# Kernel tuning notes

Hardware: AMD Instinct MI355X
Metric: run time of the kernel (lower is better)

## Reference

```python
import jax, jax.numpy as jnp
import numpy as np

B, N, D = 8, 2048, 1024

def setup_inputs() -> dict:
    key = jax.random.key(0)
    k1, k2, k3, k4 = jax.random.split(key, 4)
    q = jax.random.normal(k1, (B, N, D), dtype=jnp.float32)
    k = jax.random.normal(k2, (B, N, D), dtype=jnp.float32)
    v = jax.random.uniform(k3, (B, N, N), dtype=jnp.float32)
    # nn.Linear default init (kaiming-uniform-ish); scale is irrelevant for correctness
    bound = 1.0 / np.sqrt(D)
    W1 = jax.random.uniform(k4, (D, D), dtype=jnp.float32, minval=-bound, maxval=bound)
    b1 = jnp.zeros((D,), dtype=jnp.float32)
    return {"q": q, "k": k, "v": v, "W1": W1, "b1": b1}

def adj_normalization(adj):
    # D^{-1/2} A D^{-1/2} with rowsum clamped at 1; expressed as O(N^2)
    # broadcast scaling instead of the original's two diagonal bmms.
    rowsum = jnp.maximum(adj.sum(-1), 1.0)          # [B, N]
    d_inv_sqrt = rowsum ** -0.5                      # [B, N]
    return d_inv_sqrt[:, :, None] * adj * d_inv_sqrt[:, None, :]

def reference(q, k, v, W1, b1):
    # ff_layers == 1: q_out = linear1(q) (dropout is identity in eval);
    # k is unused because _fc returns (q_out, q_out).
    q_out = jnp.einsum('bnd,ed->bne', q, W1) + b1    # [B, N, D]
    attn = jnp.einsum('bnd,bmd->bnm', q_out, q_out)  # [B, N, N]
    # comb_mode == 2 (learn_n_norm): symmetric normalization of attn; v unused.
    output = adj_normalization(attn)
    return (output, attn)
```

## Files before the change

### kernel.cpp

```cpp
#include <hip/hip_runtime.h>

#define B_ 8
#define N_ 2048
#define D_ 1024

using u16 = unsigned short;
typedef __attribute__((ext_vector_type(8))) short short8;
typedef __attribute__((ext_vector_type(4))) float f32x4;
typedef __attribute__((ext_vector_type(4))) float float4v;
typedef __attribute__((ext_vector_type(4))) int int4v;

static __device__ __forceinline__ float bf2f(u16 h) {
  return __uint_as_float(((unsigned)h) << 16);
}
static __device__ __forceinline__ u16 f2bf(float f) {
  unsigned u = __float_as_uint(f);
  u += 0x7FFFu + ((u >> 16) & 1u);
  return (u16)(u >> 16);
}

static __device__ __forceinline__ void gload16(const void* g, void* l) {
  __builtin_amdgcn_global_load_lds((const __attribute__((address_space(1))) void*)g,
                                   (__attribute__((address_space(3))) void*)l, 16, 0, 0);
}


__device__ __forceinline__ void stage(u16* __restrict__ L,
                                      const u16* __restrict__ gA,
                                      const u16* __restrict__ gB,
                                      int kof, int w) {
  #pragma unroll
  for (int i = 0; i < 4; ++i)
    gload16(gA + (size_t)(i * 64) * 1024 + kof, L + i * 4096 + w * 512);
  #pragma unroll
  for (int i = 0; i < 4; ++i)
    gload16(gB + (size_t)(i * 64) * 1024 + kof, L + 16384 + i * 4096 + w * 512);
}

__device__ __forceinline__ void ktile(const u16* __restrict__ Lb,
                                      int wr, int wc, int lane15, int ck0,
                                      f32x4 (&acc)[8][4]) {
  const u16* Ar = Lb + (wr * 128 + lane15) * 64;
  const u16* Br = Lb + 16384 + (wc * 64 + lane15) * 64;
  const int ck1 = ck0 ^ 32;
  short8 a[4], a2[4], b[4];

  #pragma unroll
  for (int m = 0; m < 4; ++m) a[m] = *(const short8*)(Ar + m * 1024 + ck0);
  #pragma unroll
  for (int n = 0; n < 4; ++n) b[n] = *(const short8*)(Br + n * 1024 + ck0);
  __builtin_amdgcn_s_barrier();
  __builtin_amdgcn_s_setprio(1);
  #pragma unroll
  for (int m = 0; m < 4; ++m)
    #pragma unroll
    for (int n = 0; n < 4; ++n)
      acc[m][n] = __builtin_amdgcn_mfma_f32_16x16x32_bf16(a[m], b[n], acc[m][n], 0, 0, 0);
  __builtin_amdgcn_s_setprio(0);
  __builtin_amdgcn_s_barrier();

  #pragma unroll
  for (int m = 0; m < 4; ++m) a2[m] = *(const short8*)(Ar + (m + 4) * 1024 + ck0);
  __builtin_amdgcn_s_barrier();
  __builtin_amdgcn_s_setprio(1);
  #pragma unroll
  for (int m = 0; m < 4; ++m)
    #pragma unroll
    for (int n = 0; n < 4; ++n)
      acc[m + 4][n] = __builtin_amdgcn_mfma_f32_16x16x32_bf16(a2[m], b[n], acc[m + 4][n], 0, 0, 0);
  __builtin_amdgcn_s_setprio(0);
  __builtin_amdgcn_s_barrier();

  #pragma unroll
  for (int m = 0; m < 4; ++m) a[m] = *(const short8*)(Ar + m * 1024 + ck1);
  #pragma unroll
  for (int n = 0; n < 4; ++n) b[n] = *(const short8*)(Br + n * 1024 + ck1);
  __builtin_amdgcn_s_barrier();
  __builtin_amdgcn_s_setprio(1);
  #pragma unroll
  for (int m = 0; m < 4; ++m)
    #pragma unroll
    for (int n = 0; n < 4; ++n)
      acc[m][n] = __builtin_amdgcn_mfma_f32_16x16x32_bf16(a[m], b[n], acc[m][n], 0, 0, 0);
  __builtin_amdgcn_s_setprio(0);
  __builtin_amdgcn_s_barrier();

  #pragma unroll
  for (int m = 0; m < 4; ++m) a2[m] = *(const short8*)(Ar + (m + 4) * 1024 + ck1);
  __builtin_amdgcn_s_barrier();
  __builtin_amdgcn_s_setprio(1);
  #pragma unroll
  for (int m = 0; m < 4; ++m)
    #pragma unroll
    for (int n = 0; n < 4; ++n)
      acc[m + 4][n] = __builtin_amdgcn_mfma_f32_16x16x32_bf16(a2[m], b[n], acc[m + 4][n], 0, 0, 0);
  __builtin_amdgcn_s_setprio(0);
  __builtin_amdgcn_s_barrier();
}

template<int MODE>
__global__ __launch_bounds__(512, 2)
void gemm8p(const u16* __restrict__ Abase, const u16* __restrict__ Bbase,
            const float* __restrict__ aux,
            void* __restrict__ C0, float* __restrict__ C1)
{
  __shared__ u16 lds[2][32768];
  const int tid = threadIdx.x;
  const int w = tid >> 6, l = tid & 63;

  int tm0, tn0, z = 0;
  if (MODE == 0) {
    const int bid = blockIdx.x;
    const int s = (bid & 7) * 32 + (bid >> 3);
    tm0 = (s >> 2) << 8;
    tn0 = (s & 3) << 8;
  } else {
    const int bid = blockIdx.x;
    const int s = (bid & 7) * 64 + (bid >> 3);
    z  = s >> 6;
    tm0 = ((s >> 3) & 7) << 8;
    tn0 = (s & 7) << 8;
  }
  const u16* A  = Abase + (MODE ? (size_t)z * N_ * D_ : 0);
  const u16* Bm = (MODE ? A : Bbase);

  const int sr = w * 8 + (l >> 3);
  const int sc = (((l & 7) ^ (l >> 3)) << 4) >> 1;
  const u16* gA = A  + (size_t)(tm0 + sr) * 1024 + sc;
  const u16* gB = Bm + (size_t)(tn0 + sr) * 1024 + sc;

  const int lane15 = l & 15, lhi = l >> 4;
  const int ck0 = ((lhi << 4) ^ ((l & 7) << 4)) >> 1;
  const int wr = w >> 2, wc = w & 3;

  f32x4 acc[8][4];
  #pragma unroll
  for (int m = 0; m < 8; ++m)
    #pragma unroll
    for (int n = 0; n < 4; ++n)
      acc[m][n] = (f32x4){0.f, 0.f, 0.f, 0.f};

  stage(&lds[0][0], gA, gB, 0, w);
  stage(&lds[1][0], gA, gB, 64, w);

  for (int t = 0; t < 16; t += 2) {
    asm volatile("s_waitcnt vmcnt(8)" ::: "memory");
    __builtin_amdgcn_s_barrier();
    ktile(&lds[0][0], wr, wc, lane15, ck0, acc);
    stage(&lds[0][0], gA, gB, ((t + 2) & 15) * 64, w);
    asm volatile("s_waitcnt vmcnt(8)" ::: "memory");
    __builtin_amdgcn_s_barrier();
    ktile(&lds[1][0], wr, wc, lane15, ck0, acc);
    stage(&lds[1][0], gA, gB, ((t + 3) & 15) * 64, w);
  }
  asm volatile("s_waitcnt vmcnt(0)" ::: "memory");

  const int rbase = tm0 + wr * 128 + lhi * 4;
  const int cbase = tn0 + wc * 64 + lane15;

  if (MODE == 0) {
    u16* C = (u16*)C0;
    #pragma unroll
    for (int m = 0; m < 8; ++m)
      #pragma unroll
      for (int n = 0; n < 4; ++n) {
        const int col = cbase + n * 16;
        const float bv = aux[col];
        #pragma unroll
        for (int j = 0; j < 4; ++j)
          C[(size_t)(rbase + m * 16 + j) * 1024 + col] = f2bf(acc[m][n][j] + bv);
      }
  } else {
    float* Cattn = (float*)C0 + (size_t)z * N_ * N_;
    float* Cout  = C1 + (size_t)z * N_ * N_;
    const float* dv = aux + z * N_;
    float di[8][4];
    #pragma unroll
    for (int m = 0; m < 8; ++m)
      #pragma unroll
      for (int j = 0; j < 4; ++j)
        di[m][j] = dv[rbase + m * 16 + j];
    #pragma unroll
    for (int m = 0; m < 8; ++m)
      #pragma unroll
      for (int n = 0; n < 4; ++n) {
        const int col = cbase + n * 16;
        const float dj = dv[col];
        #pragma unroll
        for (int j = 0; j < 4; ++j) {
          const size_t off = (size_t)(rbase + m * 16 + j) * N_ + col;
          const float a = acc[m][n][j];
          Cattn[off] = a;
          Cout[off]  = a * di[m][j] * dj;
        }
      }
  }
}

__global__ void cvt_q_qsum(const float* __restrict__ q, u16* __restrict__ qbf,
                           float* __restrict__ qsum) {
  const int wi = blockIdx.x * 256 + threadIdx.x;
  const int d0 = (wi & 127) * 8;
  const int rc = (wi >> 7) & 63;
  const int b  = wi >> 13;
  const size_t base = ((size_t)b * N_ + rc * 32) * D_ + d0;
  float s[8];
  #pragma unroll
  for (int k = 0; k < 8; ++k) s[k] = 0.f;
  for (int r = 0; r < 32; ++r) {
    const float4v* p = (const float4v*)(q + base + (size_t)r * D_);
    float4v x = p[0], y = p[1];
    union { u16 h[8]; int4v v; } o;
    o.h[0] = f2bf(x.x); o.h[1] = f2bf(x.y); o.h[2] = f2bf(x.z); o.h[3] = f2bf(x.w);
    o.h[4] = f2bf(y.x); o.h[5] = f2bf(y.y); o.h[6] = f2bf(y.z); o.h[7] = f2bf(y.w);
    *(int4v*)(qbf + base + (size_t)r * D_) = o.v;
    s[0] += x.x; s[1] += x.y; s[2] += x.z; s[3] += x.w;
    s[4] += y.x; s[5] += y.y; s[6] += y.z; s[7] += y.w;
  }
  float* qs = qsum + b * D_ + d0;
  #pragma unroll
  for (int k = 0; k < 8; ++k) atomicAdd(qs + k, s[k]);
}

__global__ void cvt_f32_to_bf16(const float* __restrict__ in, u16* __restrict__ out, int n8) {
  const int stride = gridDim.x * blockDim.x;
  for (int i = blockIdx.x * blockDim.x + threadIdx.x; i < n8; i += stride) {
    const float4v* p = (const float4v*)in + (size_t)i * 2;
    float4v a = p[0], b = p[1];
    union { u16 h[8]; int4v v; } r;
    r.h[0] = f2bf(a.x); r.h[1] = f2bf(a.y); r.h[2] = f2bf(a.z); r.h[3] = f2bf(a.w);
    r.h[4] = f2bf(b.x); r.h[5] = f2bf(b.y); r.h[6] = f2bf(b.z); r.h[7] = f2bf(b.w);
    ((int4v*)out)[i] = r.v;
  }
}

__global__ void s_kernel(const float* __restrict__ qsum, const float* __restrict__ W1,
                         const float* __restrict__ b1, float* __restrict__ s) {
  const int idx = blockIdx.x * 256 + threadIdx.x;
  const int b = idx >> 10, e = idx & (D_ - 1);
  const int d0 = blockIdx.y * 256;
  const float4v* wp = (const float4v*)(W1 + (size_t)e * D_ + d0);
  const float4v* qp = (const float4v*)(qsum + b * D_ + d0);
  float acc = 0.f;
  #pragma unroll 4
  for (int t = 0; t < 64; ++t) {
    float4v wv = wp[t], qv = qp[t];
    acc += wv.x * qv.x + wv.y * qv.y + wv.z * qv.z + wv.w * qv.w;
  }
  if (blockIdx.y == 0) acc += (float)N_ * b1[e];
  atomicAdd(&s[b * D_ + e], acc);
}

__global__ void t_kernel(const float* __restrict__ W1, const float* __restrict__ s,
                         float* __restrict__ tv) {
  const int idx = blockIdx.x * 256 + threadIdx.x;
  const int b = idx >> 10, d = idx & (D_ - 1);
  const int e0 = blockIdx.y * 256;
  const float* wp = W1 + (size_t)e0 * D_ + d;
  const float* sp = s + b * D_ + e0;
  float acc = 0.f;
  #pragma unroll 8
  for (int e = 0; e < 256; ++e) acc += wp[(size_t)e * D_] * sp[e];
  atomicAdd(&tv[b * D_ + d], acc);
}

__global__ void c_kernel(const float* __restrict__ b1, const float* __restrict__ s,
                         float* __restrict__ c) {
  const int b = blockIdx.x;
  const int tid = threadIdx.x;
  float acc = 0.f;
  #pragma unroll
  for (int t = 0; t < 4; ++t) {
    const int e = tid + t * 256;
    acc += b1[e] * s[b * D_ + e];
  }
  __shared__ float red[4];
  #pragma unroll
  for (int off = 32; off; off >>= 1) acc += __shfl_down(acc, off);
  if ((tid & 63) == 0) red[tid >> 6] = acc;
  __syncthreads();
  if (tid == 0) c[b] = red[0] + red[1] + red[2] + red[3];
}

__global__ void rowdinv_kernel(const float* __restrict__ q, const float* __restrict__ tv,
                               const float* __restrict__ c, float* __restrict__ dinv) {
  const int row  = blockIdx.x * 4 + (threadIdx.x >> 6);
  const int lane = threadIdx.x & 63;
  const int b    = row >> 11;
  const float4v* p  = (const float4v*)(q + (size_t)row * D_);
  const float4v* tp = (const float4v*)(tv + b * D_);
  float acc = 0.f;
  #pragma unroll
  for (int it = 0; it < 4; ++it) {
    float4v qv = p[it * 64 + lane];
    float4v tw = tp[it * 64 + lane];
    acc += qv.x * tw.x + qv.y * tw.y + qv.z * tw.z + qv.w * tw.w;
  }
  #pragma unroll
  for (int off = 32; off; off >>= 1) acc += __shfl_down(acc, off);
  if (lane == 0) dinv[row] = rsqrtf(fmaxf(acc + c[b], 1.0f));
}

extern "C" void kernel_launch(void* const* d_in, const int* in_sizes, int n_in,
                              void* d_out, int out_size, void* d_ws, size_t ws_size,
                              hipStream_t stream) {
  const float* q  = (const float*)d_in[0];
  const float* W1 = (const float*)d_in[3];
  const float* b1 = (const float*)d_in[4];

  float* out  = (float*)d_out;
  float* attn = out + (size_t)B_ * N_ * N_;

  char* ws = (char*)d_ws;
  u16*   qbf  = (u16*)ws;
  u16*   qout = (u16*)(ws + (size_t)33554432);
  u16*   w1bf = (u16*)(ws + (size_t)67108864);
  float* qsum = (float*)(ws + (size_t)69206016);
  float* s    = (float*)(ws + (size_t)69238784);
  float* tv   = (float*)(ws + (size_t)69271552);
  float* c    = (float*)(ws + (size_t)69304320);
  float* dinv = (float*)(ws + (size_t)69304576);

  hipMemsetAsync(qsum, 0, 3 * B_ * D_ * sizeof(float) + 256, stream);

  cvt_q_qsum<<<256, 256, 0, stream>>>(q, qbf, qsum);
  cvt_f32_to_bf16<<<512, 256, 0, stream>>>(W1, w1bf, D_ * D_ / 8);

  gemm8p<0><<<256, 512, 0, stream>>>(qbf, w1bf, b1, qout, nullptr);

  s_kernel<<<dim3(B_ * D_ / 256, 4), 256, 0, stream>>>(qsum, W1, b1, s);
  t_kernel<<<dim3(B_ * D_ / 256, 4), 256, 0, stream>>>(W1, s, tv);
  c_kernel<<<B_, 256, 0, stream>>>(b1, s, c);
  rowdinv_kernel<<<(B_ * N_) / 4, 256, 0, stream>>>(q, tv, c, dinv);

  gemm8p<1><<<512, 512, 0, stream>>>(qout, nullptr, dinv, attn, out);
}
```

Before: 216.3 us.

## Interleave per-slab global-to-LDS prefetch with MFMA phases in GEMM mainloop

Restructures the GEMM mainloop so the next k-tile is loaded slab by slab between the four MFMA phases of the current tile, with a finer vmcnt wait, in place of staging a whole tile after compute. The MFMA phase order is changed so B fragments for both k-halves are reused across the M halves, and the first A slabs of the following tile are prefetched into the buffer just consumed. Separately, the q-conversion, s and t reduction kernels get more blocks with less work each, to raise parallelism on the small prep kernels. The finer interleaving makes buffer-reuse hazards harder to get right and adds more atomics in the prep kernels.

```diff
diff --git a/kernel.cpp b/kernel.cpp
--- a/kernel.cpp
+++ b/kernel.cpp
@@ -24,76 +24,82 @@
                                    (__attribute__((address_space(3))) void*)l, 16, 0, 0);
 }
 
-
-__device__ __forceinline__ void stage(u16* __restrict__ L,
-                                      const u16* __restrict__ gA,
-                                      const u16* __restrict__ gB,
-                                      int kof, int w) {
-  #pragma unroll
-  for (int i = 0; i < 4; ++i)
-    gload16(gA + (size_t)(i * 64) * 1024 + kof, L + i * 4096 + w * 512);
-  #pragma unroll
-  for (int i = 0; i < 4; ++i)
-    gload16(gB + (size_t)(i * 64) * 1024 + kof, L + 16384 + i * 4096 + w * 512);
-}
-
-__device__ __forceinline__ void ktile(const u16* __restrict__ Lb,
-                                      int wr, int wc, int lane15, int ck0,
-                                      f32x4 (&acc)[8][4]) {
-  const u16* Ar = Lb + (wr * 128 + lane15) * 64;
-  const u16* Br = Lb + 16384 + (wc * 64 + lane15) * 64;
+static __device__ __forceinline__ void stage_slab(u16* __restrict__ L,
+                                                  const u16* __restrict__ g,
+                                                  int slab, int kof, int w) {
+  gload16(g + (size_t)(slab * 64) * 1024 + kof, L + slab * 4096 + w * 512);
+}
+
+
+template<int S1, int S2, int VM>
+__device__ __forceinline__ void tile_body(u16* __restrict__ cur, u16* __restrict__ nxt,
+                                          const u16* __restrict__ gA, const u16* __restrict__ gB,
+                                          int kn1, int kn2,
+                                          int w, int wr, int wc, int lane15, int ck0,
+                                          f32x4 (&acc)[8][4])
+{
+  const u16* Ar = cur + (wr * 128 + lane15) * 64;
+  const u16* Br = cur + 16384 + (wc * 64 + lane15) * 64;
   const int ck1 = ck0 ^ 32;
-  short8 a[4], a2[4], b[4];
+  short8 a[4], bk0[4], bk1[4];
+
+  if constexpr (VM == 2) asm volatile("s_waitcnt vmcnt(2)" ::: "memory");
+  else                   asm volatile("s_waitcnt vmcnt(0)" ::: "memory");
+  __builtin_amdgcn_s_barrier();
 
   #pragma unroll
   for (int m = 0; m < 4; ++m) a[m] = *(const short8*)(Ar + m * 1024 + ck0);
   #pragma unroll
-  for (int n = 0; n < 4; ++n) b[n] = *(const short8*)(Br + n * 1024 + ck0);
+  for (int n = 0; n < 4; ++n) bk0[n] = *(const short8*)(Br + n * 1024 + ck0);
+  if constexpr (S1) { stage_slab(nxt, gA, 1, kn1, w); stage_slab(nxt, gA, 3, kn1, w); }
   __builtin_amdgcn_s_barrier();
   __builtin_amdgcn_s_setprio(1);
   #pragma unroll
   for (int m = 0; m < 4; ++m)
     #pragma unroll
     for (int n = 0; n < 4; ++n)
-      acc[m][n] = __builtin_amdgcn_mfma_f32_16x16x32_bf16(a[m], b[n], acc[m][n], 0, 0, 0);
+      acc[m][n] = __builtin_amdgcn_mfma_f32_16x16x32_bf16(a[m], bk0[n], acc[m][n], 0, 0, 0);
   __builtin_amdgcn_s_setprio(0);
   __builtin_amdgcn_s_barrier();
 
   #pragma unroll
-  for (int m = 0; m < 4; ++m) a2[m] = *(const short8*)(Ar + (m + 4) * 1024 + ck0);
+  for (int m = 0; m < 4; ++m) a[m] = *(const short8*)(Ar + m * 1024 + ck1);
+  #pragma unroll
+  for (int n = 0; n < 4; ++n) bk1[n] = *(const short8*)(Br + n * 1024 + ck1);
+  if constexpr (S1) { stage_slab(nxt + 16384, gB, 0, kn1, w); stage_slab(nxt + 16384, gB, 1, kn1, w); }
   __builtin_amdgcn_s_barrier();
   __builtin_amdgcn_s_setprio(1);
   #pragma unroll
   for (int m = 0; m < 4; ++m)
     #pragma unroll
     for (int n = 0; n < 4; ++n)
-      acc[m + 4][n] = __builtin_amdgcn_mfma_f32_16x16x32_bf16(a2[m], b[n], acc[m + 4][n], 0, 0, 0);
+      acc[m][n] = __builtin_amdgcn_mfma_f32_16x16x32_bf16(a[m], bk1[n], acc[m][n], 0, 0, 0);
   __builtin_amdgcn_s_setprio(0);
   __builtin_amdgcn_s_barrier();
 
   #pragma unroll
-  for (int m = 0; m < 4; ++m) a[m] = *(const short8*)(Ar + m * 1024 + ck1);
-  #pragma unroll
-  for (int n = 0; n < 4; ++n) b[n] = *(const short8*)(Br + n * 1024 + ck1);
+  for (int m = 0; m < 4; ++m) a[m] = *(const short8*)(Ar + (m + 4) * 1024 + ck0);
+  if constexpr (S1) { stage_slab(nxt + 16384, gB, 2, kn1, w); stage_slab(nxt + 16384, gB, 3, kn1, w); }
   __builtin_amdgcn_s_barrier();
   __builtin_amdgcn_s_setprio(1);
   #pragma unroll
   for (int m = 0; m < 4; ++m)
     #pragma unroll
     for (int n = 0; n < 4; ++n)
-      acc[m][n] = __builtin_amdgcn_mfma_f32_16x16x32_bf16(a[m], b[n], acc[m][n], 0, 0, 0);
+      acc[m + 4][n] = __builtin_amdgcn_mfma_f32_16x16x32_bf16(a[m], bk0[n], acc[m + 4][n], 0, 0, 0);
   __builtin_amdgcn_s_setprio(0);
   __builtin_amdgcn_s_barrier();
 
   #pragma unroll
-  for (int m = 0; m < 4; ++m) a2[m] = *(const short8*)(Ar + (m + 4) * 1024 + ck1);
+  for (int m = 0; m < 4; ++m) a[m] = *(const short8*)(Ar + (m + 4) * 1024 + ck1);
+  if constexpr (S2) { stage_slab(cur, gA, 0, kn2, w); stage_slab(cur, gA, 2, kn2, w); }
   __builtin_amdgcn_s_barrier();
   __builtin_amdgcn_s_setprio(1);
   #pragma unroll
   for (int m = 0; m < 4; ++m)
     #pragma unroll
     for (int n = 0; n < 4; ++n)
-      acc[m + 4][n] = __builtin_amdgcn_mfma_f32_16x16x32_bf16(a2[m], b[n], acc[m + 4][n], 0, 0, 0);
+      acc[m + 4][n] = __builtin_amdgcn_mfma_f32_16x16x32_bf16(a[m], bk1[n], acc[m + 4][n], 0, 0, 0);
   __builtin_amdgcn_s_setprio(0);
   __builtin_amdgcn_s_barrier();
 }
@@ -124,8 +130,8 @@
   const u16* A  = Abase + (MODE ? (size_t)z * N_ * D_ : 0);
   const u16* Bm = (MODE ? A : Bbase);
 
+  const int sc = (((l & 7) ^ (l >> 3)) << 4) >> 1;
   const int sr = w * 8 + (l >> 3);
-  const int sc = (((l & 7) ^ (l >> 3)) << 4) >> 1;
   const u16* gA = A  + (size_t)(tm0 + sr) * 1024 + sc;
   const u16* gB = Bm + (size_t)(tn0 + sr) * 1024 + sc;
 
@@ -140,19 +146,24 @@
     for (int n = 0; n < 4; ++n)
       acc[m][n] = (f32x4){0.f, 0.f, 0.f, 0.f};
 
-  stage(&lds[0][0], gA, gB, 0, w);
-  stage(&lds[1][0], gA, gB, 64, w);
-
-  for (int t = 0; t < 16; t += 2) {
-    asm volatile("s_waitcnt vmcnt(8)" ::: "memory");
-    __builtin_amdgcn_s_barrier();
-    ktile(&lds[0][0], wr, wc, lane15, ck0, acc);
-    stage(&lds[0][0], gA, gB, ((t + 2) & 15) * 64, w);
-    asm volatile("s_waitcnt vmcnt(8)" ::: "memory");
-    __builtin_amdgcn_s_barrier();
-    ktile(&lds[1][0], wr, wc, lane15, ck0, acc);
-    stage(&lds[1][0], gA, gB, ((t + 3) & 15) * 64, w);
-  }
+  u16* cur = &lds[0][0];
+  u16* nxt = &lds[1][0];
+
+  #pragma unroll
+  for (int s4 = 0; s4 < 4; ++s4) stage_slab(cur, gA, s4, 0, w);
+  #pragma unroll
+  for (int s4 = 0; s4 < 4; ++s4) stage_slab(cur + 16384, gB, s4, 0, w);
+  stage_slab(nxt, gA, 0, 64, w);
+  stage_slab(nxt, gA, 2, 64, w);
+
+  for (int t = 0; t < 14; ++t) {
+    tile_body<1, 1, 2>(cur, nxt, gA, gB, (t + 1) * 64, (t + 2) * 64,
+                       w, wr, wc, lane15, ck0, acc);
+    u16* tmp = cur; cur = nxt; nxt = tmp;
+  }
+  tile_body<1, 0, 2>(cur, nxt, gA, gB, 15 * 64, 0, w, wr, wc, lane15, ck0, acc);
+  { u16* tmp = cur; cur = nxt; nxt = tmp; }
+  tile_body<0, 0, 0>(cur, nxt, gA, gB, 0, 0, w, wr, wc, lane15, ck0, acc);
   asm volatile("s_waitcnt vmcnt(0)" ::: "memory");
 
   const int rbase = tm0 + wr * 128 + lhi * 4;
@@ -201,13 +212,14 @@
                            float* __restrict__ qsum) {
   const int wi = blockIdx.x * 256 + threadIdx.x;
   const int d0 = (wi & 127) * 8;
-  const int rc = (wi >> 7) & 63;
-  const int b  = wi >> 13;
-  const size_t base = ((size_t)b * N_ + rc * 32) * D_ + d0;
+  const int rc = (wi >> 7) & 127;
+  const int b  = wi >> 14;
+  const size_t base = ((size_t)b * N_ + rc * 16) * D_ + d0;
   float s[8];
   #pragma unroll
   for (int k = 0; k < 8; ++k) s[k] = 0.f;
-  for (int r = 0; r < 32; ++r) {
+  #pragma unroll 4
+  for (int r = 0; r < 16; ++r) {
     const float4v* p = (const float4v*)(q + base + (size_t)r * D_);
     float4v x = p[0], y = p[1];
     union { u16 h[8]; int4v v; } o;
@@ -238,12 +250,12 @@
                          const float* __restrict__ b1, float* __restrict__ s) {
   const int idx = blockIdx.x * 256 + threadIdx.x;
   const int b = idx >> 10, e = idx & (D_ - 1);
-  const int d0 = blockIdx.y * 256;
+  const int d0 = blockIdx.y * 64;
   const float4v* wp = (const float4v*)(W1 + (size_t)e * D_ + d0);
   const float4v* qp = (const float4v*)(qsum + b * D_ + d0);
   float acc = 0.f;
   #pragma unroll 4
-  for (int t = 0; t < 64; ++t) {
+  for (int t = 0; t < 16; ++t) {
     float4v wv = wp[t], qv = qp[t];
     acc += wv.x * qv.x + wv.y * qv.y + wv.z * qv.z + wv.w * qv.w;
   }
@@ -255,12 +267,12 @@
                          float* __restrict__ tv) {
   const int idx = blockIdx.x * 256 + threadIdx.x;
   const int b = idx >> 10, d = idx & (D_ - 1);
-  const int e0 = blockIdx.y * 256;
+  const int e0 = blockIdx.y * 64;
   const float* wp = W1 + (size_t)e0 * D_ + d;
   const float* sp = s + b * D_ + e0;
   float acc = 0.f;
   #pragma unroll 8
-  for (int e = 0; e < 256; ++e) acc += wp[(size_t)e * D_] * sp[e];
+  for (int e = 0; e < 64; ++e) acc += wp[(size_t)e * D_] * sp[e];
   atomicAdd(&tv[b * D_ + d], acc);
 }
 
@@ -323,13 +335,13 @@
 
   hipMemsetAsync(qsum, 0, 3 * B_ * D_ * sizeof(float) + 256, stream);
 
-  cvt_q_qsum<<<256, 256, 0, stream>>>(q, qbf, qsum);
+  cvt_q_qsum<<<512, 256, 0, stream>>>(q, qbf, qsum);
   cvt_f32_to_bf16<<<512, 256, 0, stream>>>(W1, w1bf, D_ * D_ / 8);
 
   gemm8p<0><<<256, 512, 0, stream>>>(qbf, w1bf, b1, qout, nullptr);
 
-  s_kernel<<<dim3(B_ * D_ / 256, 4), 256, 0, stream>>>(qsum, W1, b1, s);
-  t_kernel<<<dim3(B_ * D_ / 256, 4), 256, 0, stream>>>(W1, s, tv);
+  s_kernel<<<dim3(B_ * D_ / 256, 16), 256, 0, stream>>>(qsum, W1, b1, s);
+  t_kernel<<<dim3(B_ * D_ / 256, 16), 256, 0, stream>>>(W1, s, tv);
   c_kernel<<<B_, 256, 0, stream>>>(b1, s, c);
   rowdinv_kernel<<<(B_ * N_) / 4, 256, 0, stream>>>(q, tv, c, dinv);
 
```

After: 217.1 us. No clear change (+0.4%).
